# Performance work log

Hardware: AMD Instinct MI355X
Metric: run time of the kernel (lower is better)

Reference implementation:

```python
import jax, jax.numpy as jnp
import numpy as np

N_NODES = 100000
N_EDGES = 1600000
N_FEATS = 128
HIDDEN = 20
N_GRAPHS = 256
N_CLASSES = 2


def setup_inputs() -> dict:
    key = jax.random.key(0)
    ks = jax.random.split(key, 12)
    x = jax.random.normal(ks[0], (N_NODES, N_FEATS), dtype=jnp.float32)
    edge_index = jax.random.randint(ks[1], (2, N_EDGES), 0, N_NODES, dtype=jnp.int64)
    batch = jnp.sort(jax.random.randint(ks[2], (N_NODES,), 0, N_GRAPHS, dtype=jnp.int64))
    def lin_init(k, fan_in, fan_out):
        kw, kb = jax.random.split(k)
        bound = 1.0 / np.sqrt(fan_in)
        W = jax.random.uniform(kw, (fan_in, fan_out), minval=-bound, maxval=bound, dtype=jnp.float32)
        b = jax.random.uniform(kb, (fan_out,), minval=-bound, maxval=bound, dtype=jnp.float32)
        return W, b
    W1, b1 = lin_init(ks[3], N_FEATS, HIDDEN)
    W2, b2 = lin_init(ks[4], HIDDEN, HIDDEN)
    W3, b3 = lin_init(ks[5], HIDDEN, HIDDEN)
    Wl, bl = lin_init(ks[6], 2 * HIDDEN, N_CLASSES)
    return {"x": x, "edge_index": edge_index, "batch": batch,
            "W1": W1, "b1": b1, "W2": W2, "b2": b2, "W3": W3, "b3": b3,
            "Wl": Wl, "bl": bl}


def gin_conv(x, src, dst, W, b):
    # GINConv with eps=0: mlp((1+eps)*x + sum_{j in N(i)} x_j)
    agg = jax.ops.segment_sum(x[src], dst, num_segments=x.shape[0])
    return (x + agg) @ W + b


def reference(x, edge_index, batch, W1, b1, W2, b2, W3, b3, Wl, bl):
    src, dst = edge_index[0], edge_index[1]
    h = jax.nn.relu(gin_conv(x, src, dst, W1, b1))
    h = jax.nn.relu(gin_conv(h, src, dst, W2, b2))
    h = jax.nn.relu(gin_conv(h, src, dst, W3, b3))  # [N, HIDDEN]
    # global max / mean pool per graph
    out1 = jax.ops.segment_max(h, batch, num_segments=N_GRAPHS)
    sums = jax.ops.segment_sum(h, batch, num_segments=N_GRAPHS)
    counts = jax.ops.segment_sum(jnp.ones((h.shape[0],), h.dtype), batch, num_segments=N_GRAPHS)
    out2 = sums / jnp.maximum(counts, 1.0)[:, None]
    pooled = jnp.concatenate([out1, out2], axis=-1)  # [G, 2*HIDDEN]
    return pooled @ Wl + bl
```

## Files before the change

### kernel.cpp

```cpp
#include <hip/hip_runtime.h>
#include <hip/hip_fp16.h>
#include <math.h>

#define N_NODES 100000
#define N_EDGES 1600000
#define N_FEATS 128
#define HIDDEN 20
#define N_GRAPHS 256

#define TILE 256
#define NB ((N_NODES + TILE - 1) / TILE)
#define SLOTS 5120
#define YSTRIDE 32

__device__ __half g_yh[2][(size_t)N_NODES * YSTRIDE];
__device__ float  g_facc[(size_t)N_NODES * HIDDEN];
__device__ int    g_part[(size_t)NB * SLOTS];
__device__ int    g_cursor[NB];
__device__ int    g_bbase[NB];
__device__ int    g_rowptr[N_NODES + 1];
__device__ int    g_col[N_EDGES];

__device__ __forceinline__ int detect_is64(const int* __restrict__ e32) {
    int acc = 0;
    #pragma unroll
    for (int j = 0; j < 8; j++) {
        int k = j * (N_EDGES / 8) + 997 * j + 13;
        acc |= e32[2 * k + 1];
    }
    return acc == 0;
}

__device__ __forceinline__ void load_edge(const void* eidx, int is64, int e,
                                          int& s, int& d) {
    if (is64) {
        const long long* e64 = (const long long*)eidx;
        s = (int)e64[e];
        d = (int)e64[N_EDGES + e];
    } else {
        const int* e32 = (const int*)eidx;
        s = e32[e];
        d = e32[N_EDGES + e];
    }
}

__global__ __launch_bounds__(512) void zero_kernel() {
    const int i = threadIdx.x;
    if (i < NB) g_cursor[i] = 0;
}

__global__ __launch_bounds__(512) void part_kernel(const void* __restrict__ eidx) {
    __shared__ int hist[NB];
    __shared__ int base[NB];
    const int t = threadIdx.x;
    const int e0 = blockIdx.x * 4096;
    for (int i = t; i < NB; i += 512) hist[i] = 0;
    const int is64 = detect_is64((const int*)eidx);
    __syncthreads();

    int sc[8], dc[8];
    #pragma unroll
    for (int k = 0; k < 8; k++) {
        const int e = e0 + k * 512 + t;
        sc[k] = -1; dc[k] = 0;
        if (e < N_EDGES) {
            int s, d;
            load_edge(eidx, is64, e, s, d);
            if ((unsigned)s < N_NODES && (unsigned)d < N_NODES) {
                sc[k] = s; dc[k] = d;
                atomicAdd(&hist[d >> 8], 1);
            }
        }
    }
    __syncthreads();
    for (int b = t; b < NB; b += 512) {
        const int c = hist[b];
        base[b] = c ? atomicAdd(&g_cursor[b], c) : 0;
        hist[b] = 0;
    }
    __syncthreads();
    #pragma unroll
    for (int k = 0; k < 8; k++) {
        if (sc[k] >= 0) {
            const int b = dc[k] >> 8;
            const int r = atomicAdd(&hist[b], 1);
            const int pos = base[b] + r;
            if (pos < SLOTS)
                g_part[(size_t)b * SLOTS + pos] = (sc[k] << 8) | (dc[k] & 255);
        }
    }
}

__global__ __launch_bounds__(512) void scanbase_kernel() {
    __shared__ int lds[512];
    const int t = threadIdx.x;
    int v = (t < NB) ? min(g_cursor[t], SLOTS) : 0;
    lds[t] = v;
    __syncthreads();
    for (int off = 1; off < 512; off <<= 1) {
        int u = (t >= off) ? lds[t - off] : 0;
        __syncthreads();
        lds[t] += u;
        __syncthreads();
    }
    if (t < NB) g_bbase[t] = lds[t] - v;
    if (t == 511) g_rowptr[N_NODES] = lds[511];
}

__global__ __launch_bounds__(512) void bucketsort_kernel() {
    __shared__ int hist[TILE];
    __shared__ int pfx[TILE];
    __shared__ int cur[TILE];
    __shared__ int sorted[SLOTS];
    const int t = threadIdx.x;
    const int b = blockIdx.x;
    const int cnt = min(g_cursor[b], SLOTS);
    const int base = g_bbase[b];
    if (t < TILE) hist[t] = 0;
    __syncthreads();
    const int* __restrict__ part = g_part + (size_t)b * SLOTS;
    for (int i = t; i < cnt; i += 512) atomicAdd(&hist[part[i] & 255], 1);
    __syncthreads();
    if (t < TILE) pfx[t] = hist[t];
    __syncthreads();
    for (int off = 1; off < TILE; off <<= 1) {
        int u = (t < TILE && t >= off) ? pfx[t - off] : 0;
        __syncthreads();
        if (t < TILE) pfx[t] += u;
        __syncthreads();
    }
    if (t < TILE) {
        const int ex = pfx[t] - hist[t];
        cur[t] = ex;
        const int node = b * TILE + t;
        if (node < N_NODES) g_rowptr[node] = base + ex;
    }
    __syncthreads();
    for (int i = t; i < cnt; i += 512) {
        const int rec = part[i];
        const int r = atomicAdd(&cur[rec & 255], 1);
        sorted[r] = rec >> 8;
    }
    __syncthreads();
    for (int i = t; i < cnt; i += 512) g_col[base + i] = sorted[i];
}

#define XSTRIDE 129
__global__ __launch_bounds__(256) void mm1_kernel(const float* __restrict__ x,
                                                  const float* __restrict__ W) {
    __shared__ float ldsW[N_FEATS * HIDDEN];
    __shared__ float ldsX[64 * XSTRIDE];
    const int t = threadIdx.x;
    for (int i = t; i < N_FEATS * HIDDEN; i += 256) ldsW[i] = W[i];
    const int rowBase = blockIdx.x * 64;
    for (int i = t; i < 64 * (N_FEATS / 4); i += 256) {
        int r = i >> 5;
        int kc = i & 31;
        float4 v = make_float4(0.f, 0.f, 0.f, 0.f);
        int grow = rowBase + r;
        if (grow < N_NODES) v = ((const float4*)x)[(size_t)grow * (N_FEATS / 4) + kc];
        float* row = &ldsX[r * XSTRIDE];
        row[0 * 32 + kc] = v.x;
        row[1 * 32 + kc] = v.y;
        row[2 * 32 + kc] = v.z;
        row[3 * 32 + kc] = v.w;
    }
    __syncthreads();
    const int r = t & 63;
    const int cbase = (t >> 6) * 5;
    float a0 = 0.f, a1 = 0.f, a2 = 0.f, a3 = 0.f, a4 = 0.f;
    const float* xrow = &ldsX[r * XSTRIDE];
    #pragma unroll 4
    for (int k = 0; k < N_FEATS; k++) {
        float xv = xrow[((k & 3) << 5) + (k >> 2)];
        const float* w = &ldsW[k * HIDDEN + cbase];
        a0 = fmaf(xv, w[0], a0);
        a1 = fmaf(xv, w[1], a1);
        a2 = fmaf(xv, w[2], a2);
        a3 = fmaf(xv, w[3], a3);
        a4 = fmaf(xv, w[4], a4);
    }
    const int grow = rowBase + r;
    if (grow < N_NODES) {
        __half* yp = &g_yh[0][(size_t)grow * YSTRIDE + cbase];
        yp[0] = __float2half_rn(a0);
        yp[1] = __float2half_rn(a1);
        yp[2] = __float2half_rn(a2);
        yp[3] = __float2half_rn(a3);
        yp[4] = __float2half_rn(a4);
    }
}

template<bool FINAL>
__global__ __launch_bounds__(320) void gt_kernel(const float* __restrict__ bias,
                                                 const float* __restrict__ W,
                                                 int src) {
    const __half* __restrict__ y = g_yh[src];
    __shared__ float hrow[64][HIDDEN + 1];
    __shared__ float ldsW[HIDDEN * HIDDEN];
    __shared__ float ldsB[HIDDEN];
    const int t = threadIdx.x;
    if (!FINAL) {
        for (int i = t; i < HIDDEN * HIDDEN; i += 320) ldsW[i] = W[i];
        if (t < HIDDEN) ldsB[t] = bias[t];
    }
    const int nl = t / 5;
    const int chunk = t - nl * 5;
    const int node = blockIdx.x * 64 + nl;
    float sx = 0.f, sy = 0.f, sz = 0.f, sw = 0.f;
    if (node < N_NODES) {
        const int beg = g_rowptr[node];
        const int end = g_rowptr[node + 1];
        const int cb = chunk * 4;
        int i = beg;
        for (; i + 4 <= end; i += 4) {
            const int s0 = g_col[i + 0];
            const int s1 = g_col[i + 1];
            const int s2 = g_col[i + 2];
            const int s3 = g_col[i + 3];
            const uint2 u0 = *(const uint2*)&y[(size_t)s0 * YSTRIDE + cb];
            const uint2 u1 = *(const uint2*)&y[(size_t)s1 * YSTRIDE + cb];
            const uint2 u2 = *(const uint2*)&y[(size_t)s2 * YSTRIDE + cb];
            const uint2 u3 = *(const uint2*)&y[(size_t)s3 * YSTRIDE + cb];
            float2 a, b;
            a = __half22float2(*(const __half2*)&u0.x); b = __half22float2(*(const __half2*)&u0.y);
            sx += a.x; sy += a.y; sz += b.x; sw += b.y;
            a = __half22float2(*(const __half2*)&u1.x); b = __half22float2(*(const __half2*)&u1.y);
            sx += a.x; sy += a.y; sz += b.x; sw += b.y;
            a = __half22float2(*(const __half2*)&u2.x); b = __half22float2(*(const __half2*)&u2.y);
            sx += a.x; sy += a.y; sz += b.x; sw += b.y;
            a = __half22float2(*(const __half2*)&u3.x); b = __half22float2(*(const __half2*)&u3.y);
            sx += a.x; sy += a.y; sz += b.x; sw += b.y;
        }
        for (; i < end; i++) {
            const int s = g_col[i];
            const uint2 u = *(const uint2*)&y[(size_t)s * YSTRIDE + cb];
            const float2 f0 = __half22float2(*(const __half2*)&u.x);
            const float2 f1 = __half22float2(*(const __half2*)&u.y);
            sx += f0.x; sy += f0.y; sz += f1.x; sw += f1.y;
        }
        const uint2 u = *(const uint2*)&y[(size_t)node * YSTRIDE + cb];
        const float2 f0 = __half22float2(*(const __half2*)&u.x);
        const float2 f1 = __half22float2(*(const __half2*)&u.y);
        sx += f0.x; sy += f0.y; sz += f1.x; sw += f1.y;
    }
    if (FINAL) {
        if (node < N_NODES) {
            float4 o; o.x = sx; o.y = sy; o.z = sz; o.w = sw;
            *(float4*)&g_facc[(size_t)node * HIDDEN + chunk * 4] = o;
        }
        return;
    }
    if (node < N_NODES) {
        hrow[nl][chunk * 4 + 0] = sx;
        hrow[nl][chunk * 4 + 1] = sy;
        hrow[nl][chunk * 4 + 2] = sz;
        hrow[nl][chunk * 4 + 3] = sw;
    }
    __syncthreads();
    if (node < N_NODES) {
        float h[HIDDEN];
        #pragma unroll
        for (int c = 0; c < HIDDEN; c++) {
            float v = hrow[nl][c] + ldsB[c];
            h[c] = v > 0.f ? v : 0.f;
        }
        const int cb = chunk * 4;
        float s0 = 0.f, s1 = 0.f, s2 = 0.f, s3 = 0.f;
        #pragma unroll
        for (int k = 0; k < HIDDEN; k++) {
            const float* w = &ldsW[k * HIDDEN + cb];
            s0 = fmaf(h[k], w[0], s0);
            s1 = fmaf(h[k], w[1], s1);
            s2 = fmaf(h[k], w[2], s2);
            s3 = fmaf(h[k], w[3], s3);
        }
        __half2 o0 = __float22half2_rn(make_float2(s0, s1));
        __half2 o1 = __float22half2_rn(make_float2(s2, s3));
        uint2 u;
        u.x = *(unsigned*)&o0;
        u.y = *(unsigned*)&o1;
        *(uint2*)&g_yh[src ^ 1][(size_t)node * YSTRIDE + cb] = u;
    }
}

__global__ __launch_bounds__(256) void pool_kernel(const float* __restrict__ b3,
                                                   const void* __restrict__ batch,
                                                   const void* __restrict__ eidx,
                                                   const float* __restrict__ Wl,
                                                   const float* __restrict__ bl,
                                                   float* __restrict__ out) {
    const float* __restrict__ acc3 = g_facc;
    const int g = blockIdx.x;
    const int t = threadIdx.x;
    const int is64 = detect_is64((const int*)eidx);
    const int* b32 = (const int*)batch;
    const long long* b64 = (const long long*)batch;
    #define BAT(i) (is64 ? (int)b64[i] : b32[i])
    int lo = 0, hi = N_NODES;
    while (lo < hi) { int mid = (lo + hi) >> 1; if (BAT(mid) < g) lo = mid + 1; else hi = mid; }
    const int start = lo;
    lo = start; hi = N_NODES;
    while (lo < hi) { int mid = (lo + hi) >> 1; if (BAT(mid) < g + 1) lo = mid + 1; else hi = mid; }
    const int end = lo;
    #undef BAT

    float b3r[HIDDEN];
    #pragma unroll
    for (int c = 0; c < HIDDEN; c++) b3r[c] = b3[c];
    float mx[HIDDEN], sm[HIDDEN];
    #pragma unroll
    for (int c = 0; c < HIDDEN; c++) { mx[c] = 0.f; sm[c] = 0.f; }

    for (int i = start + t; i < end; i += 256) {
        const float4* rp = (const float4*)&acc3[(size_t)i * HIDDEN];
        float4 q[5] = {rp[0], rp[1], rp[2], rp[3], rp[4]};
        const float* r = (const float*)q;
        #pragma unroll
        for (int c = 0; c < HIDDEN; c++) {
            float v = r[c] + b3r[c];
            v = v > 0.f ? v : 0.f;
            mx[c] = fmaxf(mx[c], v);
            sm[c] += v;
        }
    }
    #pragma unroll
    for (int off = 32; off >= 1; off >>= 1) {
        #pragma unroll
        for (int c = 0; c < HIDDEN; c++) {
            mx[c] = fmaxf(mx[c], __shfl_xor(mx[c], off));
            sm[c] += __shfl_xor(sm[c], off);
        }
    }
    __shared__ float smx[4][HIDDEN];
    __shared__ float ssm[4][HIDDEN];
    const int wave = t >> 6, lane = t & 63;
    if (lane == 0) {
        #pragma unroll
        for (int c = 0; c < HIDDEN; c++) { smx[wave][c] = mx[c]; ssm[wave][c] = sm[c]; }
    }
    __syncthreads();
    if (t == 0) {
        float cnt = (float)(end - start);
        float pooled[2 * HIDDEN];
        #pragma unroll
        for (int c = 0; c < HIDDEN; c++) {
            float m = smx[0][c], s = ssm[0][c];
            #pragma unroll
            for (int w = 1; w < 4; w++) { m = fmaxf(m, smx[w][c]); s += ssm[w][c]; }
            pooled[c] = m;
            pooled[HIDDEN + c] = s / fmaxf(cnt, 1.f);
        }
        #pragma unroll
        for (int c = 0; c < 2; c++) {
            float o = bl[c];
            #pragma unroll
            for (int k = 0; k < 2 * HIDDEN; k++) o = fmaf(pooled[k], Wl[k * 2 + c], o);
            out[g * 2 + c] = o;
        }
    }
}

extern "C" void kernel_launch(void* const* d_in, const int* in_sizes, int n_in,
                              void* d_out, int out_size, void* d_ws, size_t ws_size,
                              hipStream_t stream) {
    const float* x    = (const float*)d_in[0];
    const void* eidx  = d_in[1];
    const void* batch = d_in[2];
    const float* W1  = (const float*)d_in[3];
    const float* b1  = (const float*)d_in[4];
    const float* W2  = (const float*)d_in[5];
    const float* b2  = (const float*)d_in[6];
    const float* W3  = (const float*)d_in[7];
    const float* b3  = (const float*)d_in[8];
    const float* Wl  = (const float*)d_in[9];
    const float* bl  = (const float*)d_in[10];
    float* out = (float*)d_out;
    (void)d_ws; (void)ws_size;

    const int mm1_blocks = (N_NODES + 63) / 64;
    const int gt_blocks  = (N_NODES + 63) / 64;

    zero_kernel<<<1, 512, 0, stream>>>();
    part_kernel<<<NB, 512, 0, stream>>>(eidx);
    scanbase_kernel<<<1, 512, 0, stream>>>();
    bucketsort_kernel<<<NB, 512, 0, stream>>>();

    mm1_kernel<<<mm1_blocks, 256, 0, stream>>>(x, W1);
    gt_kernel<false><<<gt_blocks, 320, 0, stream>>>(b1, W2, 0);
    gt_kernel<false><<<gt_blocks, 320, 0, stream>>>(b2, W3, 1);
    gt_kernel<true><<<gt_blocks, 320, 0, stream>>>(nullptr, nullptr, 0);
    pool_kernel<<<N_GRAPHS, 256, 0, stream>>>(b3, batch, eidx, Wl, bl, out);
}
```

Before: 183.3 us.

## Rewrite first-layer matmul to load x directly into registers with split-K shuffle reduction

The first-layer matmul no longer stages x tiles in shared memory. Each group of four threads now handles one row, and each thread reads a contiguous 32-float chunk of that row as float4 loads straight into registers. W is permuted in LDS so each thread reads it as float4, all 20 outputs are accumulated per thread, the four partial sums are combined with xor shuffles, and the results are written to the half-precision y buffer as wide vector stores. This removes an LDS round trip and a barrier and gives the x reads and output stores better coalescing. In exchange it uses more registers (32 floats of x plus 20 accumulators) and adds shuffle-reduction work.

```diff
diff --git a/kernel.cpp b/kernel.cpp
--- a/kernel.cpp
+++ b/kernel.cpp
@@ -145,49 +145,85 @@
     for (int i = t; i < cnt; i += 512) g_col[base + i] = sorted[i];
 }
 
-#define XSTRIDE 129
 __global__ __launch_bounds__(256) void mm1_kernel(const float* __restrict__ x,
                                                   const float* __restrict__ W) {
-    __shared__ float ldsW[N_FEATS * HIDDEN];
-    __shared__ float ldsX[64 * XSTRIDE];
-    const int t = threadIdx.x;
-    for (int i = t; i < N_FEATS * HIDDEN; i += 256) ldsW[i] = W[i];
-    const int rowBase = blockIdx.x * 64;
-    for (int i = t; i < 64 * (N_FEATS / 4); i += 256) {
-        int r = i >> 5;
-        int kc = i & 31;
-        float4 v = make_float4(0.f, 0.f, 0.f, 0.f);
-        int grow = rowBase + r;
-        if (grow < N_NODES) v = ((const float4*)x)[(size_t)grow * (N_FEATS / 4) + kc];
-        float* row = &ldsX[r * XSTRIDE];
-        row[0 * 32 + kc] = v.x;
-        row[1 * 32 + kc] = v.y;
-        row[2 * 32 + kc] = v.z;
-        row[3 * 32 + kc] = v.w;
-    }
-    __syncthreads();
-    const int r = t & 63;
-    const int cbase = (t >> 6) * 5;
-    float a0 = 0.f, a1 = 0.f, a2 = 0.f, a3 = 0.f, a4 = 0.f;
-    const float* xrow = &ldsX[r * XSTRIDE];
-    #pragma unroll 4
-    for (int k = 0; k < N_FEATS; k++) {
-        float xv = xrow[((k & 3) << 5) + (k >> 2)];
-        const float* w = &ldsW[k * HIDDEN + cbase];
-        a0 = fmaf(xv, w[0], a0);
-        a1 = fmaf(xv, w[1], a1);
-        a2 = fmaf(xv, w[2], a2);
-        a3 = fmaf(xv, w[3], a3);
-        a4 = fmaf(xv, w[4], a4);
-    }
-    const int grow = rowBase + r;
-    if (grow < N_NODES) {
-        __half* yp = &g_yh[0][(size_t)grow * YSTRIDE + cbase];
-        yp[0] = __float2half_rn(a0);
-        yp[1] = __float2half_rn(a1);
-        yp[2] = __float2half_rn(a2);
-        yp[3] = __float2half_rn(a3);
-        yp[4] = __float2half_rn(a4);
+    __shared__ float ldsWp[N_FEATS * HIDDEN];
+    const int t = threadIdx.x;
+    for (int i = t; i < N_FEATS * HIDDEN; i += 256) {
+        const int korig = i / HIDDEN;
+        const int c = i - korig * HIDDEN;
+        const int jl = korig & 31;
+        const int q = korig >> 5;
+        ldsWp[(jl * 4 + q) * HIDDEN + c] = W[i];
+    }
+    __syncthreads();
+    const int r = t >> 2;
+    const int q = t & 3;
+    const int row = blockIdx.x * 64 + r;
+    const bool valid = row < N_NODES;
+
+    float4 v[8];
+    if (valid) {
+        const float4* rp = (const float4*)&x[(size_t)row * N_FEATS + q * 32];
+        #pragma unroll
+        for (int i = 0; i < 8; i++) v[i] = rp[i];
+    }
+    float4 a0 = {0,0,0,0}, a1 = {0,0,0,0}, a2 = {0,0,0,0}, a3 = {0,0,0,0}, a4 = {0,0,0,0};
+    if (valid) {
+        #pragma unroll
+        for (int i = 0; i < 8; i++) {
+            const float xv[4] = {v[i].x, v[i].y, v[i].z, v[i].w};
+            #pragma unroll
+            for (int jj = 0; jj < 4; jj++) {
+                const int jl = i * 4 + jj;
+                const float4* wp = (const float4*)&ldsWp[(jl * 4 + q) * HIDDEN];
+                const float xs = xv[jj];
+                float4 w0 = wp[0], w1 = wp[1], w2 = wp[2], w3 = wp[3], w4 = wp[4];
+                a0.x = fmaf(xs, w0.x, a0.x); a0.y = fmaf(xs, w0.y, a0.y);
+                a0.z = fmaf(xs, w0.z, a0.z); a0.w = fmaf(xs, w0.w, a0.w);
+                a1.x = fmaf(xs, w1.x, a1.x); a1.y = fmaf(xs, w1.y, a1.y);
+                a1.z = fmaf(xs, w1.z, a1.z); a1.w = fmaf(xs, w1.w, a1.w);
+                a2.x = fmaf(xs, w2.x, a2.x); a2.y = fmaf(xs, w2.y, a2.y);
+                a2.z = fmaf(xs, w2.z, a2.z); a2.w = fmaf(xs, w2.w, a2.w);
+                a3.x = fmaf(xs, w3.x, a3.x); a3.y = fmaf(xs, w3.y, a3.y);
+                a3.z = fmaf(xs, w3.z, a3.z); a3.w = fmaf(xs, w3.w, a3.w);
+                a4.x = fmaf(xs, w4.x, a4.x); a4.y = fmaf(xs, w4.y, a4.y);
+                a4.z = fmaf(xs, w4.z, a4.z); a4.w = fmaf(xs, w4.w, a4.w);
+            }
+        }
+    }
+    float acc[20] = {a0.x, a0.y, a0.z, a0.w, a1.x, a1.y, a1.z, a1.w,
+                     a2.x, a2.y, a2.z, a2.w, a3.x, a3.y, a3.z, a3.w,
+                     a4.x, a4.y, a4.z, a4.w};
+    #pragma unroll
+    for (int off = 1; off <= 2; off <<= 1) {
+        #pragma unroll
+        for (int c = 0; c < 20; c++) acc[c] += __shfl_xor(acc[c], off);
+    }
+    if (valid) {
+        __half* yp = &g_yh[0][(size_t)row * YSTRIDE];
+        if (q == 0) {
+            __half2 h0 = __float22half2_rn(make_float2(acc[0], acc[1]));
+            __half2 h1 = __float22half2_rn(make_float2(acc[2], acc[3]));
+            __half2 h2 = __float22half2_rn(make_float2(acc[4], acc[5]));
+            __half2 h3 = __float22half2_rn(make_float2(acc[6], acc[7]));
+            uint4 u; u.x = *(unsigned*)&h0; u.y = *(unsigned*)&h1;
+            u.z = *(unsigned*)&h2; u.w = *(unsigned*)&h3;
+            *(uint4*)&yp[0] = u;
+        } else if (q == 1) {
+            __half2 h0 = __float22half2_rn(make_float2(acc[8], acc[9]));
+            __half2 h1 = __float22half2_rn(make_float2(acc[10], acc[11]));
+            __half2 h2 = __float22half2_rn(make_float2(acc[12], acc[13]));
+            __half2 h3 = __float22half2_rn(make_float2(acc[14], acc[15]));
+            uint4 u; u.x = *(unsigned*)&h0; u.y = *(unsigned*)&h1;
+            u.z = *(unsigned*)&h2; u.w = *(unsigned*)&h3;
+            *(uint4*)&yp[8] = u;
+        } else if (q == 2) {
+            __half2 h0 = __float22half2_rn(make_float2(acc[16], acc[17]));
+            __half2 h1 = __float22half2_rn(make_float2(acc[18], acc[19]));
+            uint2 u; u.x = *(unsigned*)&h0; u.y = *(unsigned*)&h1;
+            *(uint2*)&yp[16] = u;
+        }
     }
 }
 
```

Measured after the change: 173.8 us. 1.05x faster.
